# Performance work log

Hardware: AMD Instinct MI355X
Metric: run time of the kernel (lower is better)

Reference implementation:

```python
import jax, jax.numpy as jnp
import numpy as np

INTERVAL = 8
HEADS = 4
DIM = 64


def grid_shuffle(x, I):
    # rearrange 'b c (h i) (w j) -> (b i j) c h w' : stride-I residue grouping
    B, C, H, W = x.shape
    h, w = H // I, W // I
    x = x.reshape(B, C, h, I, w, I).transpose(0, 3, 5, 1, 2, 4)
    return x.reshape(B * I * I, C, h, w)


def grid_unshuffle(x, I, B):
    Bp, C, h, w = x.shape
    x = x.reshape(B, I, I, C, h, w).transpose(0, 3, 4, 1, 5, 2)
    return x.reshape(B, C, h * I, w * I)


def conv1x1(x, w, b):
    return jnp.einsum('oc,bchw->bohw', w, x) + b[None, :, None, None]


def pos_bias(h, w, W1, b1, W2, b2):
    # dynamic RPE: MLP over normalized relative coordinates -> [heads, N, N]
    ch = jnp.arange(h)
    cw = jnp.arange(w)
    coords = jnp.stack(jnp.meshgrid(ch, cw, indexing='ij'), -1).reshape(-1, 2).astype(jnp.float32)
    denom = jnp.array([max(h - 1, 1), max(w - 1, 1)], dtype=jnp.float32)
    rel = (coords[:, None, :] - coords[None, :, :]) / denom  # [N,N,2]
    hid = jax.nn.relu(rel @ W1 + b1)
    bias = hid @ W2 + b2  # [N,N,heads]
    return bias.transpose(2, 0, 1)


def mask_attn(q2d, k2d, v2d, bias, pw, pb, heads, scale):
    Bp, C, h, w = q2d.shape
    N, d = h * w, C // heads

    def to_tok(t):  # [Bp,C,h,w] -> [Bp,heads,N,d]
        return t.reshape(Bp, heads, d, N).transpose(0, 1, 3, 2)

    q, k, v = to_tok(q2d), to_tok(k2d), to_tok(v2d)
    attn = jnp.einsum('bhnd,bhmd->bhnm', q * scale, k) + bias[None]
    attn = jax.nn.softmax(attn, axis=-1)
    out = jnp.einsum('bhnm,bhmd->bhnd', attn, v)
    out2d = out.transpose(0, 1, 3, 2).reshape(Bp, C, h, w)
    return conv1x1(out2d, pw, pb)


def setup_inputs() -> dict:
    key = jax.random.key(0)
    ks = jax.random.split(key, 14)
    pos_hidden = DIM // 4  # 16
    s = 0.02
    return {
        'x': jax.random.normal(ks[0], (2, DIM, 160, 160), jnp.float32),
        'qkv_w': jax.random.normal(ks[1], (3 * DIM, DIM), jnp.float32) * s,
        'qkv_b': jnp.zeros((3 * DIM,), jnp.float32),
        'grid_w': jax.random.normal(ks[2], (DIM, DIM), jnp.float32) * s,
        'grid_b': jnp.zeros((DIM,), jnp.float32),
        'pos_w1': jax.random.normal(ks[3], (2, pos_hidden), jnp.float32) * s,
        'pos_b1': jnp.zeros((pos_hidden,), jnp.float32),
        'pos_w2': jax.random.normal(ks[4], (pos_hidden, HEADS), jnp.float32) * s,
        'pos_b2': jnp.zeros((HEADS,), jnp.float32),
        'proj1_w': jax.random.normal(ks[5], (DIM, DIM), jnp.float32) * s,
        'proj1_b': jnp.zeros((DIM,), jnp.float32),
        'proj2_w': jax.random.normal(ks[6], (DIM, DIM), jnp.float32) * s,
        'proj2_b': jnp.zeros((DIM,), jnp.float32),
    }


def reference(x, qkv_w, qkv_b, grid_w, grid_b, pos_w1, pos_b1, pos_w2, pos_b2,
              proj1_w, proj1_b, proj2_w, proj2_b):
    I = INTERVAL
    scale = (DIM // HEADS) ** -0.5
    B, C, H, W = x.shape
    qkv = conv1x1(x, qkv_w, qkv_b)
    x_grid = conv1x1(grid_shuffle(x, I), grid_w, grid_b)
    qkv = grid_shuffle(qkv, I)
    bias = pos_bias(H // I, W // I, pos_w1, pos_b1, pos_w2, pos_b2)
    q, k, v = jnp.split(qkv, 3, axis=1)
    out = mask_attn(x_grid, k, v, bias, proj1_w, proj1_b, HEADS, scale)
    out = mask_attn(q, x_grid, out, bias, proj2_w, proj2_b, HEADS, scale)
    return grid_unshuffle(out, I, B)
```

## Files before the change

### kernel.cpp

```cpp
#include <hip/hip_runtime.h>
#include <hip/hip_bf16.h>


#define N_TOK 400
#define NP    416
#define BP    128

typedef short bf16x8 __attribute__((ext_vector_type(8)));
typedef float f32x16 __attribute__((ext_vector_type(16)));

__device__ inline ushort f2bf(float f) {
    __hip_bfloat16 h = __float2bfloat16(f);
    return *reinterpret_cast<ushort*>(&h);
}
__device__ inline float bf2f(ushort u) {
    union { uint i; float f; } v; v.i = (uint)u << 16; return v.f;
}
__device__ inline uint pk2(float a, float b) {
    return (uint)f2bf(a) | ((uint)f2bf(b) << 16);
}
__device__ inline bf16x8 ld16(const ushort* p) {
    union { uint4 q; bf16x8 v; } u;
    u.q = *reinterpret_cast<const uint4*>(p);
    return u.v;
}
__device__ inline float fast_exp2(float x) {
#if __has_builtin(__builtin_amdgcn_exp2f)
    return __builtin_amdgcn_exp2f(x);
#else
    return __expf(x * 0.6931471805599453f);
#endif
}

#define L2E 1.4426950408889634f

__global__ __launch_bounds__(256) void k_prep(
    const float* __restrict__ W1, const float* __restrict__ B1,
    const float* __restrict__ W2, const float* __restrict__ B2,
    const float* __restrict__ qkv_w, const float* __restrict__ qkv_b,
    const float* __restrict__ grid_w, const float* __restrict__ grid_b,
    const float* __restrict__ p1w, const float* __restrict__ p2w,
    float* __restrict__ biasF, ushort* __restrict__ Wc, float* __restrict__ Bc,
    ushort* __restrict__ Wp1, ushort* __restrict__ Wp2)
{
    int blk = blockIdx.x;
    if (blk < 2704) {
        int idx = blk * 256 + threadIdx.x;
        if (idx >= 692224) return;
        int r = idx & 15, lane = (idx >> 4) & 63;
        int tile = idx >> 10;
        int mt = tile % 13, rem = tile / 13, qt = rem % 13, h = rem / 13;
        int n = qt * 32 + (lane & 31);
        int m = mt * 32 + (r & 3) + 8 * (r >> 2) + 4 * (lane >> 5);
        float val = 0.0f;
        if (n < 400 && m < 400) {
            float r0 = (float)(n / 20 - m / 20) * (1.0f / 19.0f);
            float r1 = (float)(n % 20 - m % 20) * (1.0f / 19.0f);
            float o = B2[h];
#pragma unroll
            for (int k = 0; k < 16; ++k) {
                float hh = r0 * W1[k] + r1 * W1[16 + k] + B1[k];
                hh = fmaxf(hh, 0.0f);
                o += hh * W2[k * 4 + h];
            }
            val = 4.0f * o;
        }
        biasF[idx] = val;
    } else {
        int t = (blk - 2704) * 256 + threadIdx.x;
        if (t < 16384) {
            int oc = t >> 6, k = t & 63;
            float v = (oc < 192) ? qkv_w[oc * 64 + k] : grid_w[(oc - 192) * 64 + k];
            Wc[t] = f2bf(v);
        } else if (t < 16384 + 4096) {
            Wp1[t - 16384] = f2bf(p1w[t - 16384]);
        } else if (t < 16384 + 8192) {
            Wp2[t - 16384 - 4096] = f2bf(p2w[t - 16384 - 4096]);
        } else if (t < 16384 + 8192 + 256) {
            int oc = t - 16384 - 8192;
            Bc[oc] = (oc < 192) ? qkv_b[oc] : grid_b[oc - 192];
        }
    }
}

__global__ __launch_bounds__(256) void k_conv(
    const float* __restrict__ x, const ushort* __restrict__ Wc,
    const float* __restrict__ Bc,
    ushort* __restrict__ Qb, ushort* __restrict__ Kb,
    ushort* __restrict__ Vb, ushort* __restrict__ XGb)
{
    __shared__ __align__(16) ushort XL[32 * 64];
    int blk = blockIdx.x;
    int b = blk / 800, rem = blk % 800;
    int H0 = rem / 5, wt = rem % 5;
    int w0 = wt * 32;
    int tid = threadIdx.x;

    {
        int c = tid >> 2, q4 = tid & 3;
        const float* xr = x + ((size_t)(b * 64 + c) * 160 + H0) * 160 + w0 + q4 * 8;
        float4 f0 = *reinterpret_cast<const float4*>(xr);
        float4 f1 = *reinterpret_cast<const float4*>(xr + 4);
        char* base = reinterpret_cast<char*>(XL);
#pragma unroll
        for (int k = 0; k < 8; ++k) {
            float v = (k < 4) ? ((const float*)&f0)[k] : ((const float*)&f1)[k - 4];
            int p = q4 * 8 + k;
            int byt = p * 128 + ((2 * c) ^ ((p & 7) << 4));
            *reinterpret_cast<ushort*>(base + byt) = f2bf(v);
        }
    }

    int lane = tid & 63, w = tid >> 6;
    int l31 = lane & 31, hi = lane >> 5;

    bf16x8 wf[2][4];
#pragma unroll
    for (int nt = 0; nt < 2; ++nt)
#pragma unroll
        for (int kk = 0; kk < 4; ++kk)
            wf[nt][kk] = ld16(&Wc[(size_t)(w * 64 + nt * 32 + l31) * 64 + kk * 16 + hi * 8]);
    __syncthreads();

    f32x16 acc0 = 0.0f, acc1 = 0.0f;
    const char* base = reinterpret_cast<const char*>(XL);
#pragma unroll
    for (int kk = 0; kk < 4; ++kk) {
        int byt = l31 * 128 + (((kk * 32 + hi * 16)) ^ ((l31 & 7) << 4));
        bf16x8 xf;
        {
            union { uint4 q; bf16x8 v; } u;
            u.q = *reinterpret_cast<const uint4*>(base + byt);
            xf = u.v;
        }
        acc0 = __builtin_amdgcn_mfma_f32_32x32x16_bf16(wf[0][kk], xf, acc0, 0, 0, 0);
        acc1 = __builtin_amdgcn_mfma_f32_32x32x16_bf16(wf[1][kk], xf, acc1, 0, 0, 0);
    }

    int W0 = w0 + l31, ww = W0 >> 3, j = W0 & 7;
    int bp = b * 64 + (H0 & 7) * 8 + j;
    int n  = (H0 >> 3) * 20 + ww;
    ushort* outb = (w == 0) ? Qb : (w == 1) ? Kb : (w == 2) ? Vb : XGb;
    ushort* dst = outb + ((size_t)bp * NP + n) * 64;
#pragma unroll
    for (int nt = 0; nt < 2; ++nt) {
        const f32x16& a = nt ? acc1 : acc0;
#pragma unroll
        for (int g = 0; g < 4; ++g) {
            int cc = nt * 32 + 8 * g + 4 * hi;
            int oc = w * 64 + cc;
            uint2 uu;
            uu.x = pk2(a[4 * g + 0] + Bc[oc + 0], a[4 * g + 1] + Bc[oc + 1]);
            uu.y = pk2(a[4 * g + 2] + Bc[oc + 2], a[4 * g + 3] + Bc[oc + 3]);
            *reinterpret_cast<uint2*>(dst + cc) = uu;
        }
    }
}

__global__ __launch_bounds__(512, 8) void k_attn_mfma(
    const ushort* __restrict__ Qg, const ushort* __restrict__ Kg,
    const ushort* __restrict__ Vg, const float* __restrict__ biasF,
    ushort* __restrict__ O, float scale2)
{
    __shared__ ushort Ks[NP * 16];
    __shared__ ushort Vt[16 * 424];
    int blk = blockIdx.x;
    int bp = blk >> 3, h = (blk >> 1) & 3, sub = blk & 1;
    int qt0 = sub ? 7 : 0;
    int cnt = sub ? 6 : 7;
    int tid = threadIdx.x;

    const ushort* Ksrc = Kg + (size_t)bp * NP * 64 + h * 16;
#pragma unroll
    for (int it = 0; it < 2; ++it) {
        int i = tid + it * 512;
        if (i < NP * 2) {
            int row = i >> 1, half = i & 1;
            *reinterpret_cast<uint4*>(&Ks[row * 16 + half * 8]) =
                *reinterpret_cast<const uint4*>(&Ksrc[(size_t)row * 64 + half * 8]);
        }
    }
    const ushort* Vsrc = Vg + (size_t)bp * NP * 64 + h * 16;
#pragma unroll
    for (int it = 0; it < 2; ++it) {
        int i = tid + it * 512;
        if (i < 800) {
            int row = i >> 1, hf = i & 1;
            uint4 v = *reinterpret_cast<const uint4*>(&Vsrc[(size_t)row * 64 + hf * 8]);
            const ushort* pv = reinterpret_cast<const ushort*>(&v);
#pragma unroll
            for (int k = 0; k < 8; ++k)
                Vt[(hf * 8 + k) * 424 + row] = pv[k];
        }
    }
    __syncthreads();

    int lane = tid & 63, w = tid >> 6;
    int l31 = lane & 31, hi = lane >> 5;

    if (w < cnt) {
        int qt = qt0 + w;
        int qbase = qt * 32;
        bf16x8 qf = ld16(&Qg[((size_t)bp * NP + qbase + l31) * 64 + h * 16 + hi * 8]);
        f32x16 acc = 0.0f;
        float lrun = 0.0f;
        const float* bfr = biasF + ((size_t)(h * 169 + qt * 13)) * 1024 + lane * 16;

#pragma unroll
        for (int mt = 0; mt < 13; ++mt) {
            const int mbase = mt * 32;
            bf16x8 kf = ld16(&Ks[(mbase + l31) * 16 + hi * 8]);

            union { float4 f4[4]; f32x16 v; } cb;
            const float4* bx = reinterpret_cast<const float4*>(bfr + (size_t)mt * 1024);
            cb.f4[0] = bx[0]; cb.f4[1] = bx[1]; cb.f4[2] = bx[2]; cb.f4[3] = bx[3];
            f32x16 sv = __builtin_amdgcn_mfma_f32_32x32x16_bf16(kf, qf, cb.v, 0, 0, 0);

            const int nv = (mt == 12) ? 8 : 16;
            float p[16];
#pragma unroll
            for (int r = 0; r < 16; ++r)
                if (r < nv) p[r] = fast_exp2(sv[r] * scale2);
            {
                float a = (p[0] + p[1]) + (p[2] + p[3]);
                float b = (p[4] + p[5]) + (p[6] + p[7]);
                float rs = a + b;
                if (nv == 16) {
                    float c = (p[8] + p[9]) + (p[10] + p[11]);
                    float d = (p[12] + p[13]) + (p[14] + p[15]);
                    rs += c + d;
                }
                lrun += rs;
            }

            {
                uint c4 = pk2(p[0], p[1]), c5 = pk2(p[2], p[3]);
                uint c6 = pk2(p[4], p[5]), c7 = pk2(p[6], p[7]);
                asm("v_permlane32_swap_b32 %0, %1" : "+v"(c4), "+v"(c6));
                asm("v_permlane32_swap_b32 %0, %1" : "+v"(c5), "+v"(c7));
                union { uint u[4]; bf16x8 v; } A;
                A.u[0] = c4; A.u[1] = c5; A.u[2] = c6; A.u[3] = c7;
                bf16x8 vf = ld16(&Vt[(lane & 15) * 424 + mbase + hi * 8]);
                acc = __builtin_amdgcn_mfma_f32_32x32x16_bf16(A.v, vf, acc, 0, 0, 0);
            }
            if (mt < 12) {
                uint c4 = pk2(p[8], p[9]),  c5 = pk2(p[10], p[11]);
                uint c6 = pk2(p[12], p[13]), c7 = pk2(p[14], p[15]);
                asm("v_permlane32_swap_b32 %0, %1" : "+v"(c4), "+v"(c6));
                asm("v_permlane32_swap_b32 %0, %1" : "+v"(c5), "+v"(c7));
                union { uint u[4]; bf16x8 v; } A;
                A.u[0] = c4; A.u[1] = c5; A.u[2] = c6; A.u[3] = c7;
                bf16x8 vf = ld16(&Vt[(lane & 15) * 424 + mbase + 16 + hi * 8]);
                acc = __builtin_amdgcn_mfma_f32_32x32x16_bf16(A.v, vf, acc, 0, 0, 0);
            }
        }

        float tot = lrun + __shfl_xor(lrun, 32);
        float inv = 1.0f / tot;
#pragma unroll
        for (int r = 0; r < 16; ++r) {
            int moff = (r & 3) + 8 * (r >> 2) + 4 * hi;
            int q = qbase + moff;
            float iv = __shfl(inv, moff);
            if (l31 < 16 && q < N_TOK)
                O[((size_t)bp * 400 + q) * 64 + h * 16 + l31] = f2bf(acc[r] * iv);
        }
    }
}

template<int MODE>
__global__ __launch_bounds__(256) void k_proj(
    const ushort* __restrict__ In, const ushort* __restrict__ Wp,
    const float* __restrict__ Bv, ushort* __restrict__ Out)
{
    __shared__ __align__(16) ushort XL[128 * 64];
    size_t t0 = (size_t)blockIdx.x * 128;
    int tid = threadIdx.x;

    char* basec = reinterpret_cast<char*>(XL);
#pragma unroll
    for (int it = 0; it < 4; ++it) {
        int idx = tid + it * 256;
        int p = idx >> 3, c8 = idx & 7;
        uint4 v = *reinterpret_cast<const uint4*>(In + (t0 + p) * 64 + c8 * 8);
        int byt = p * 128 + ((c8 * 16) ^ ((p & 7) << 4));
        *reinterpret_cast<uint4*>(basec + byt) = v;
    }

    int lane = tid & 63, w = tid >> 6;
    int l31 = lane & 31, hi = lane >> 5;

    bf16x8 wf[2][4];
#pragma unroll
    for (int nt = 0; nt < 2; ++nt)
#pragma unroll
        for (int kk = 0; kk < 4; ++kk)
            wf[nt][kk] = ld16(&Wp[(size_t)(nt * 32 + l31) * 64 + kk * 16 + hi * 8]);
    __syncthreads();

    int prow = w * 32 + l31;
    f32x16 acc0 = 0.0f, acc1 = 0.0f;
#pragma unroll
    for (int kk = 0; kk < 4; ++kk) {
        int byt = prow * 128 + (((kk * 32 + hi * 16)) ^ ((prow & 7) << 4));
        union { uint4 q; bf16x8 v; } u;
        u.q = *reinterpret_cast<const uint4*>(basec + byt);
        acc0 = __builtin_amdgcn_mfma_f32_32x32x16_bf16(wf[0][kk], u.v, acc0, 0, 0, 0);
        acc1 = __builtin_amdgcn_mfma_f32_32x32x16_bf16(wf[1][kk], u.v, acc1, 0, 0, 0);
    }

    size_t t = t0 + prow;
    ushort* dst;
    if (MODE == 0) {
        int bp = (int)(t / 400), n = (int)(t % 400);
        dst = Out + ((size_t)bp * NP + n) * 64;
    } else {
        dst = Out + t * 64;
    }
#pragma unroll
    for (int nt = 0; nt < 2; ++nt) {
        const f32x16& a = nt ? acc1 : acc0;
#pragma unroll
        for (int g = 0; g < 4; ++g) {
            int cc = nt * 32 + 8 * g + 4 * hi;
            uint2 uu;
            uu.x = pk2(a[4 * g + 0] + Bv[cc + 0], a[4 * g + 1] + Bv[cc + 1]);
            uu.y = pk2(a[4 * g + 2] + Bv[cc + 2], a[4 * g + 3] + Bv[cc + 3]);
            *reinterpret_cast<uint2*>(dst + cc) = uu;
        }
    }
}

__global__ __launch_bounds__(256) void k_unshuffle(
    const ushort* __restrict__ In, float* __restrict__ out)
{
    __shared__ __align__(16) ushort il[160 * 64];
    int blk = blockIdx.x;
    int b = blk / 160, rem = blk % 160, iI = rem / 20, hh = rem % 20;
    int tid = threadIdx.x;

    for (int idx = tid; idx < 1280; idx += 256) {
        int j = idx / 160, r2 = idx % 160, ww = r2 / 8, c8 = r2 % 8;
        int bp = b * 64 + iI * 8 + j;
        int n  = hh * 20 + ww;
        uint4 v = reinterpret_cast<const uint4*>(In + ((size_t)bp * 400 + n) * 64)[c8];
        reinterpret_cast<uint4*>(&il[(ww * 8 + j) * 64])[c8] = v;
    }
    __syncthreads();

    int c = tid >> 2, q = tid & 3;
    int H0 = hh * 8 + iI;
    float* og = out + ((size_t)(b * 64 + c) * 160 + H0) * 160;
#pragma unroll
    for (int k = 0; k < 10; ++k) {
        int f = q + 4 * k;
        float4 v;
        v.x = bf2f(il[(4 * f + 0) * 64 + c]);
        v.y = bf2f(il[(4 * f + 1) * 64 + c]);
        v.z = bf2f(il[(4 * f + 2) * 64 + c]);
        v.w = bf2f(il[(4 * f + 3) * 64 + c]);
        reinterpret_cast<float4*>(og)[f] = v;
    }
}

extern "C" void kernel_launch(void* const* d_in, const int* in_sizes, int n_in,
                              void* d_out, int out_size, void* d_ws, size_t ws_size,
                              hipStream_t stream)
{
    const float* x      = (const float*)d_in[0];
    const float* qkv_w  = (const float*)d_in[1];
    const float* qkv_b  = (const float*)d_in[2];
    const float* grid_w = (const float*)d_in[3];
    const float* grid_b = (const float*)d_in[4];
    const float* pw1    = (const float*)d_in[5];
    const float* pb1    = (const float*)d_in[6];
    const float* pw2    = (const float*)d_in[7];
    const float* pb2    = (const float*)d_in[8];
    const float* p1w    = (const float*)d_in[9];
    const float* p1b    = (const float*)d_in[10];
    const float* p2w    = (const float*)d_in[11];
    const float* p2b    = (const float*)d_in[12];

    char* W = (char*)d_ws;
    float*  biasF = (float*)(W + 0);
    ushort* Wc    = (ushort*)(W + 2768896);
    ushort* Wp1   = (ushort*)(W + 2801664);
    ushort* Wp2   = (ushort*)(W + 2809856);
    float*  Bc    = (float*) (W + 2818048);
    const size_t BASE2 = 2819072;
    const size_t BB = (size_t)BP * NP * 64 * 2;
    ushort* Qb = (ushort*)(W + BASE2);
    ushort* Kb = (ushort*)(W + BASE2 + 1 * BB);
    ushort* Vb = (ushort*)(W + BASE2 + 2 * BB);
    ushort* XG = (ushort*)(W + BASE2 + 3 * BB);
    ushort* P1 = (ushort*)(W + BASE2 + 4 * BB);
    const size_t OB = (size_t)BP * 400 * 64 * 2;
    ushort* O1 = (ushort*)(W + BASE2 + 5 * BB);
    ushort* O2 = (ushort*)(W + BASE2 + 5 * BB + OB);
    ushort* OFb = O1;
    float*  out = (float*)d_out;

    const float scale2 = 0.25f * L2E;

    k_prep<<<2801, 256, 0, stream>>>(pw1, pb1, pw2, pb2, qkv_w, qkv_b, grid_w, grid_b,
                                     p1w, p2w, biasF, Wc, Bc, Wp1, Wp2);
    k_conv<<<1600, 256, 0, stream>>>(x, Wc, Bc, Qb, Kb, Vb, XG);
    k_attn_mfma<<<1024, 512, 0, stream>>>(XG, Kb, Vb, biasF, O1, scale2);
    k_proj<0><<<400, 256, 0, stream>>>(O1, Wp1, p1b, P1);
    k_attn_mfma<<<1024, 512, 0, stream>>>(Qb, XG, P1, biasF, O2, scale2);
    k_proj<1><<<400, 256, 0, stream>>>(O2, Wp2, p2b, OFb);
    k_unshuffle<<<320, 256, 0, stream>>>(OFb, out);
}
```

Before: 132.2 us.

## Fold softmax scale into Q/K, compute row sums via MFMA, merge attention blocks

The softmax scale and log2(e) are folded into the Q/K projection output and the precomputed bias, which removes the per-element multiply before exp2. The row-sum adds are replaced by feeding a constant 1.0 as V in the unused 16 output columns of the PV MFMA; the denominator is then read with a shuffle and an approximate reciprocal. Each block now covers all 13 query tiles of one (batch, head) pair, with waves looping over tiles, so K/V are staged into shared memory once rather than twice. The next bias tile is prefetched into registers and the launch-bounds occupancy hint is lowered. The risks are load imbalance, since five of the eight waves process two tiles, and a small bf16 rounding difference from scaling Q/K before the conversion.

```diff
diff --git a/kernel.cpp b/kernel.cpp
--- a/kernel.cpp
+++ b/kernel.cpp
@@ -31,8 +31,16 @@
     return __expf(x * 0.6931471805599453f);
 #endif
 }
+__device__ inline float fast_rcp(float x) {
+#if __has_builtin(__builtin_amdgcn_rcpf)
+    return __builtin_amdgcn_rcpf(x);
+#else
+    return 1.0f / x;
+#endif
+}
 
 #define L2E 1.4426950408889634f
+#define QK_PRESCALE 0.36067376022224085f
 
 __global__ __launch_bounds__(256) void k_prep(
     const float* __restrict__ W1, const float* __restrict__ B1,
@@ -63,7 +71,7 @@
                 hh = fmaxf(hh, 0.0f);
                 o += hh * W2[k * 4 + h];
             }
-            val = 4.0f * o;
+            val = o * L2E;
         }
         biasF[idx] = val;
     } else {
@@ -141,6 +149,7 @@
     int bp = b * 64 + (H0 & 7) * 8 + j;
     int n  = (H0 >> 3) * 20 + ww;
     ushort* outb = (w == 0) ? Qb : (w == 1) ? Kb : (w == 2) ? Vb : XGb;
+    float mul = (w <= 1) ? QK_PRESCALE : 1.0f;
     ushort* dst = outb + ((size_t)bp * NP + n) * 64;
 #pragma unroll
     for (int nt = 0; nt < 2; ++nt) {
@@ -150,24 +159,22 @@
             int cc = nt * 32 + 8 * g + 4 * hi;
             int oc = w * 64 + cc;
             uint2 uu;
-            uu.x = pk2(a[4 * g + 0] + Bc[oc + 0], a[4 * g + 1] + Bc[oc + 1]);
-            uu.y = pk2(a[4 * g + 2] + Bc[oc + 2], a[4 * g + 3] + Bc[oc + 3]);
+            uu.x = pk2((a[4 * g + 0] + Bc[oc + 0]) * mul, (a[4 * g + 1] + Bc[oc + 1]) * mul);
+            uu.y = pk2((a[4 * g + 2] + Bc[oc + 2]) * mul, (a[4 * g + 3] + Bc[oc + 3]) * mul);
             *reinterpret_cast<uint2*>(dst + cc) = uu;
         }
     }
 }
 
-__global__ __launch_bounds__(512, 8) void k_attn_mfma(
+__global__ __launch_bounds__(512, 4) void k_attn_mfma(
     const ushort* __restrict__ Qg, const ushort* __restrict__ Kg,
     const ushort* __restrict__ Vg, const float* __restrict__ biasF,
-    ushort* __restrict__ O, float scale2)
+    ushort* __restrict__ O)
 {
     __shared__ ushort Ks[NP * 16];
     __shared__ ushort Vt[16 * 424];
     int blk = blockIdx.x;
-    int bp = blk >> 3, h = (blk >> 1) & 3, sub = blk & 1;
-    int qt0 = sub ? 7 : 0;
-    int cnt = sub ? 6 : 7;
+    int bp = blk >> 2, h = blk & 3;
     int tid = threadIdx.x;
 
     const ushort* Ksrc = Kg + (size_t)bp * NP * 64 + h * 16;
@@ -198,40 +205,39 @@
     int lane = tid & 63, w = tid >> 6;
     int l31 = lane & 31, hi = lane >> 5;
 
-    if (w < cnt) {
-        int qt = qt0 + w;
+    for (int qt = w; qt < 13; qt += 8) {
         int qbase = qt * 32;
         bf16x8 qf = ld16(&Qg[((size_t)bp * NP + qbase + l31) * 64 + h * 16 + hi * 8]);
         f32x16 acc = 0.0f;
-        float lrun = 0.0f;
         const float* bfr = biasF + ((size_t)(h * 169 + qt * 13)) * 1024 + lane * 16;
+
+        float4 cb0 = *reinterpret_cast<const float4*>(bfr + 0);
+        float4 cb1 = *reinterpret_cast<const float4*>(bfr + 4);
+        float4 cb2 = *reinterpret_cast<const float4*>(bfr + 8);
+        float4 cb3 = *reinterpret_cast<const float4*>(bfr + 12);
 
 #pragma unroll
         for (int mt = 0; mt < 13; ++mt) {
             const int mbase = mt * 32;
+            float4 nb0, nb1, nb2, nb3;
+            if (mt < 12) {
+                const float4* nx = reinterpret_cast<const float4*>(bfr + (size_t)(mt + 1) * 1024);
+                nb0 = nx[0]; nb1 = nx[1]; nb2 = nx[2]; nb3 = nx[3];
+            }
+
             bf16x8 kf = ld16(&Ks[(mbase + l31) * 16 + hi * 8]);
-
-            union { float4 f4[4]; f32x16 v; } cb;
-            const float4* bx = reinterpret_cast<const float4*>(bfr + (size_t)mt * 1024);
-            cb.f4[0] = bx[0]; cb.f4[1] = bx[1]; cb.f4[2] = bx[2]; cb.f4[3] = bx[3];
-            f32x16 sv = __builtin_amdgcn_mfma_f32_32x32x16_bf16(kf, qf, cb.v, 0, 0, 0);
+            f32x16 cin;
+            cin[0] = cb0.x; cin[1] = cb0.y; cin[2]  = cb0.z; cin[3]  = cb0.w;
+            cin[4] = cb1.x; cin[5] = cb1.y; cin[6]  = cb1.z; cin[7]  = cb1.w;
+            cin[8] = cb2.x; cin[9] = cb2.y; cin[10] = cb2.z; cin[11] = cb2.w;
+            cin[12] = cb3.x; cin[13] = cb3.y; cin[14] = cb3.z; cin[15] = cb3.w;
+            f32x16 sv = __builtin_amdgcn_mfma_f32_32x32x16_bf16(kf, qf, cin, 0, 0, 0);
 
             const int nv = (mt == 12) ? 8 : 16;
             float p[16];
 #pragma unroll
             for (int r = 0; r < 16; ++r)
-                if (r < nv) p[r] = fast_exp2(sv[r] * scale2);
-            {
-                float a = (p[0] + p[1]) + (p[2] + p[3]);
-                float b = (p[4] + p[5]) + (p[6] + p[7]);
-                float rs = a + b;
-                if (nv == 16) {
-                    float c = (p[8] + p[9]) + (p[10] + p[11]);
-                    float d = (p[12] + p[13]) + (p[14] + p[15]);
-                    rs += c + d;
-                }
-                lrun += rs;
-            }
+                if (r < nv) p[r] = fast_exp2(sv[r]);
 
             {
                 uint c4 = pk2(p[0], p[1]), c5 = pk2(p[2], p[3]);
@@ -240,7 +246,9 @@
                 asm("v_permlane32_swap_b32 %0, %1" : "+v"(c5), "+v"(c7));
                 union { uint u[4]; bf16x8 v; } A;
                 A.u[0] = c4; A.u[1] = c5; A.u[2] = c6; A.u[3] = c7;
-                bf16x8 vf = ld16(&Vt[(lane & 15) * 424 + mbase + hi * 8]);
+                bf16x8 vf;
+                if (l31 < 16) vf = ld16(&Vt[l31 * 424 + mbase + hi * 8]);
+                else { union { uint u[4]; bf16x8 v; } o; o.u[0]=o.u[1]=o.u[2]=o.u[3]=0x3F803F80u; vf = o.v; }
                 acc = __builtin_amdgcn_mfma_f32_32x32x16_bf16(A.v, vf, acc, 0, 0, 0);
             }
             if (mt < 12) {
@@ -250,20 +258,21 @@
                 asm("v_permlane32_swap_b32 %0, %1" : "+v"(c5), "+v"(c7));
                 union { uint u[4]; bf16x8 v; } A;
                 A.u[0] = c4; A.u[1] = c5; A.u[2] = c6; A.u[3] = c7;
-                bf16x8 vf = ld16(&Vt[(lane & 15) * 424 + mbase + 16 + hi * 8]);
+                bf16x8 vf;
+                if (l31 < 16) vf = ld16(&Vt[l31 * 424 + mbase + 16 + hi * 8]);
+                else { union { uint u[4]; bf16x8 v; } o; o.u[0]=o.u[1]=o.u[2]=o.u[3]=0x3F803F80u; vf = o.v; }
                 acc = __builtin_amdgcn_mfma_f32_32x32x16_bf16(A.v, vf, acc, 0, 0, 0);
             }
-        }
-
-        float tot = lrun + __shfl_xor(lrun, 32);
-        float inv = 1.0f / tot;
+            cb0 = nb0; cb1 = nb1; cb2 = nb2; cb3 = nb3;
+        }
+
 #pragma unroll
         for (int r = 0; r < 16; ++r) {
             int moff = (r & 3) + 8 * (r >> 2) + 4 * hi;
             int q = qbase + moff;
-            float iv = __shfl(inv, moff);
+            float s = __shfl(acc[r], lane | 16);
             if (l31 < 16 && q < N_TOK)
-                O[((size_t)bp * 400 + q) * 64 + h * 16 + l31] = f2bf(acc[r] * iv);
+                O[((size_t)bp * 400 + q) * 64 + h * 16 + l31] = f2bf(acc[r] * fast_rcp(s));
         }
     }
 }
@@ -400,14 +409,12 @@
     ushort* OFb = O1;
     float*  out = (float*)d_out;
 
-    const float scale2 = 0.25f * L2E;
-
     k_prep<<<2801, 256, 0, stream>>>(pw1, pb1, pw2, pb2, qkv_w, qkv_b, grid_w, grid_b,
                                      p1w, p2w, biasF, Wc, Bc, Wp1, Wp2);
     k_conv<<<1600, 256, 0, stream>>>(x, Wc, Bc, Qb, Kb, Vb, XG);
-    k_attn_mfma<<<1024, 512, 0, stream>>>(XG, Kb, Vb, biasF, O1, scale2);
+    k_attn_mfma<<<512, 512, 0, stream>>>(XG, Kb, Vb, biasF, O1);
     k_proj<0><<<400, 256, 0, stream>>>(O1, Wp1, p1b, P1);
-    k_attn_mfma<<<1024, 512, 0, stream>>>(Qb, XG, P1, biasF, O2, scale2);
+    k_attn_mfma<<<512, 512, 0, stream>>>(Qb, XG, P1, biasF, O2);
     k_proj<1><<<400, 256, 0, stream>>>(O2, Wp2, p2b, OFb);
     k_unshuffle<<<320, 256, 0, stream>>>(OFb, out);
 }
```

Result: faster. 116.0 us (-12.2%).
